# Kernel optimization log

Hardware: AMD Instinct MI355X
Metric: run time of the kernel (lower is better)

The kernel has to match this reference:

```python
import jax, jax.numpy as jnp
import numpy as np

D_MODEL = 1024
N_HEADS = 16
HEAD_DIM = D_MODEL // N_HEADS  # 64
N_T = max(1, int(N_HEADS * 0.25))  # 4 time heads
N_S = N_HEADS - N_T               # 12 space heads
T_DIM = N_T * HEAD_DIM
S_DIM = N_S * HEAD_DIM
B, L = 2, 2048


def setup_inputs() -> dict:
    key = jax.random.key(0)
    ks = jax.random.split(key, 8)
    std = 0.02
    return {
        "x": jax.random.normal(ks[0], (B, L, D_MODEL), dtype=jnp.float32),
        "attention_mask": jnp.zeros((B, 1, 1, L), dtype=jnp.float32),
        # torch nn.Linear weights have shape (out_features, in_features)
        "w_qt": jax.random.normal(ks[1], (T_DIM, D_MODEL), dtype=jnp.float32) * std,
        "w_kt": jax.random.normal(ks[2], (T_DIM, D_MODEL), dtype=jnp.float32) * std,
        "w_qs": jax.random.normal(ks[3], (S_DIM, D_MODEL), dtype=jnp.float32) * std,
        "w_ks": jax.random.normal(ks[4], (S_DIM, D_MODEL), dtype=jnp.float32) * std,
        "w_sigma": jnp.zeros((1,), dtype=jnp.float32),
        "w_v": jax.random.normal(ks[5], (D_MODEL, D_MODEL), dtype=jnp.float32) * std,
        "w_o": jax.random.normal(ks[6], (D_MODEL, D_MODEL), dtype=jnp.float32) * std,
    }


def _heads(x, w, n_h):
    # x:(B,L,D) @ w.T:(D,out) -> (B,L,n_h,d_h) -> (B,n_h,L,d_h)
    b, l, _ = x.shape
    y = jnp.einsum('bld,td->blt', x, w)
    return y.reshape(b, l, n_h, HEAD_DIM).transpose(0, 2, 1, 3)


def reference(x, attention_mask, w_qt, w_kt, w_qs, w_ks, w_sigma, w_v, w_o):
    b, l, _ = x.shape
    scale = np.sqrt(HEAD_DIM).astype(np.float32)
    # F3: time heads (sign-flipped, scaled by learnable sigma) + space heads
    Qt = _heads(x, w_qt, N_T)
    Kt = _heads(x, w_kt, N_T)
    Qs = _heads(x, w_qs, N_S)
    Ks = _heads(x, w_ks, N_S)
    st = jnp.einsum('bhqd,bhkd->bhqk', Qt, Kt)  # (B,N_T,L,L)
    ss = jnp.einsum('bhqd,bhkd->bhqk', Qs, Ks)  # (B,N_S,L,L)
    sigma = jax.nn.sigmoid(w_sigma[0])
    score = jnp.concatenate([-sigma * st, ss], axis=1) / scale  # (B,H,L,L)
    score = score + attention_mask.astype(score.dtype)
    attn_probs = jax.nn.softmax(score, axis=-1).astype(x.dtype)
    # dropout p=0.0 -> identity
    V = _heads(x, w_v, N_HEADS)  # (B,H,L,d_h)
    out = jnp.einsum('bhqk,bhkd->bhqd', attn_probs, V)
    out = out.transpose(0, 2, 1, 3).reshape(b, l, D_MODEL)
    out = jnp.einsum('bld,od->blo', out, w_o)
    return out, attn_probs
```

## Files before the change

### kernel.cpp

```cpp
#include <hip/hip_runtime.h>

typedef __bf16 bf16x8 __attribute__((ext_vector_type(8)));
typedef float f32x4 __attribute__((ext_vector_type(4)));
typedef float f32x16 __attribute__((ext_vector_type(16)));
typedef short short4v __attribute__((ext_vector_type(4)));
typedef unsigned short ushort8 __attribute__((ext_vector_type(8)));
typedef unsigned int uint4v __attribute__((ext_vector_type(4)));

#define AS1 __attribute__((address_space(1)))
#define AS3 __attribute__((address_space(3)))
#define GLL16(g, l) __builtin_amdgcn_global_load_lds((const AS1 void*)(g), (AS3 void*)(l), 16, 0, 0)
#define MFMA16(a, b, c) __builtin_amdgcn_mfma_f32_16x16x32_bf16((a), (b), (c), 0, 0, 0)
#define MFMA32(a, b, c) __builtin_amdgcn_mfma_f32_32x32x16_bf16((a), (b), (c), 0, 0, 0)
#define L2E 1.44269504f

__device__ __forceinline__ unsigned short f2bf(float f) {
  unsigned int u = __builtin_bit_cast(unsigned int, f);
  u = (u + 0x7fffu + ((u >> 16) & 1u)) >> 16;
  return (unsigned short)u;
}

__device__ __forceinline__ unsigned int cvtpk_bf16(float lo, float hi) {
  unsigned int r;
  asm("v_cvt_pk_bf16_f32 %0, %1, %2" : "=v"(r) : "v"(lo), "v"(hi));
  return r;
}

__global__ void convert_kernel(const float* __restrict__ x,
                               const float* __restrict__ w_qt, const float* __restrict__ w_kt,
                               const float* __restrict__ w_qs, const float* __restrict__ w_ks,
                               const float* __restrict__ w_v, const float* __restrict__ w_o,
                               unsigned short* __restrict__ xb, unsigned short* __restrict__ wcat,
                               unsigned short* __restrict__ wob) {
  const int NX = 4096 * 1024, NW = 3072 * 1024, NO = 1024 * 1024;
  int stride = gridDim.x * blockDim.x;
  for (int i = blockIdx.x * blockDim.x + threadIdx.x; i < NX + NW + NO; i += stride) {
    if (i < NX) {
      xb[i] = f2bf(x[i]);
    } else if (i < NX + NW) {
      int j = i - NX;
      int n = j >> 10, k = j & 1023;
      const float* src;
      if (n < 256)        src = w_qt + n * 1024;
      else if (n < 1024)  src = w_qs + (n - 256) * 1024;
      else if (n < 1280)  src = w_kt + (n - 1024) * 1024;
      else if (n < 2048)  src = w_ks + (n - 1280) * 1024;
      else                src = w_v + (n - 2048) * 1024;
      wcat[j] = f2bf(src[k]);
    } else {
      int j = i - NX - NW;
      wob[j] = f2bf(w_o[j]);
    }
  }
}

__global__ __launch_bounds__(256) void gemm_qkv(const unsigned short* __restrict__ A,
                                                const unsigned short* __restrict__ Bw,
                                                const float* __restrict__ amask,
                                                unsigned short* __restrict__ qb,
                                                unsigned short* __restrict__ kfrag,
                                                unsigned short* __restrict__ vfrag) {
  __shared__ unsigned short As[128 * 32];
  __shared__ unsigned short Bs[128 * 32];
  const int t = threadIdx.x;
  const int lane = t & 63, wid = t >> 6;
  const int wm = wid >> 1, wn = wid & 1;
  const int lr = lane & 15, lg = lane >> 4;
  const int m0 = blockIdx.x * 128, n0 = blockIdx.y * 128;
  const int K = 1024;
  f32x4 acc[4][4] = {};
  const unsigned short* gA0 = A + (m0 + (t >> 2)) * K + (t & 3) * 8;
  const unsigned short* gB0 = Bw + (n0 + (t >> 2)) * K + (t & 3) * 8;
  char* lA = (char*)As + wid * 1024;
  char* lB = (char*)Bs + wid * 1024;
  for (int k0 = 0; k0 < K; k0 += 32) {
    __syncthreads();
    GLL16(gA0 + k0, lA);
    GLL16(gA0 + 64 * K + k0, lA + 4096);
    GLL16(gB0 + k0, lB);
    GLL16(gB0 + 64 * K + k0, lB + 4096);
    __syncthreads();
    bf16x8 af[4], bfr[4];
#pragma unroll
    for (int i = 0; i < 4; ++i) {
      af[i] = *(const bf16x8*)&As[(wm * 64 + i * 16 + lr) * 32 + lg * 8];
      bfr[i] = *(const bf16x8*)&Bs[(wn * 64 + i * 16 + lr) * 32 + lg * 8];
    }
#pragma unroll
    for (int i = 0; i < 4; ++i)
#pragma unroll
      for (int j = 0; j < 4; ++j)
        acc[i][j] = MFMA16(af[i], bfr[j], acc[i][j]);
  }
#pragma unroll
  for (int i = 0; i < 4; ++i) {
#pragma unroll
    for (int j = 0; j < 4; ++j) {
      int n = n0 + wn * 64 + j * 16 + lr;
      int mb = m0 + wm * 64 + i * 16 + lg * 4;
      int b = mb >> 11, l = mb & 2047;
      f32x4 v = acc[i][j];
      if (n < 1024) {
        int h = n >> 6, d = n & 63;
#pragma unroll
        for (int r = 0; r < 4; ++r)
          qb[((b * 16 + h) * 2048 + l + r) * 64 + d] = f2bf(v[r]);
      } else if (n < 2048) {
        int nn = n - 1024;
        int h = nn >> 6, d = nn & 63;
        int mfr = d >> 4, hi2 = (d >> 3) & 1, e = d & 7;
#pragma unroll
        for (int r = 0; r < 4; ++r) {
          int lr2 = l + r;
          int cgr = lr2 >> 5, ck = lr2 & 31;
          size_t idx = ((size_t)((b * 16 + h) * 64 + cgr) * 4 + mfr) * 512 + (hi2 * 32 + ck) * 8 + e;
          kfrag[idx] = f2bf(v[r]);
        }
      } else {
        int nn = n - 2048;
        int h = nn >> 6, d = nn & 63;
        int dh = d >> 5, dcol = d & 31;
        int kk = l & 31;
        int kh = kk >> 4, hi2 = (kk >> 3) & 1, i0 = kk & 7;
        const float* mrow = amask + b * 2048 + l;
        size_t idx = ((size_t)((b * 16 + h) * 64 + (l >> 5)) * 4 + (kh * 2 + dh)) * 512
                     + (hi2 * 32 + dcol) * 8 + i0;
        short4v pk;
#pragma unroll
        for (int r = 0; r < 4; ++r)
          pk[r] = (short)f2bf(v[r] * __expf(mrow[r]));
        *(short4v*)&vfrag[idx] = pk;
      }
    }
  }
}

__global__ __launch_bounds__(256, 3) void attn_kernel(const unsigned short* __restrict__ qb,
                                                      const unsigned short* __restrict__ kfrag,
                                                      const unsigned short* __restrict__ vfrag,
                                                      const float* __restrict__ mask,
                                                      const float* __restrict__ w_sigma,
                                                      float* __restrict__ probs,
                                                      unsigned short* __restrict__ ao) {
  __shared__ __align__(16) float pvacc[2048];
  __shared__ float psum[4][32];
  __shared__ float rsum[32];
  const int t = threadIdx.x;
  const int lane = t & 63, w = t >> 6;
  const int col = lane & 31, hi = lane >> 5;
  const int s = blockIdx.x;
  const int bh = (s & 7) * 4 + ((s >> 3) >> 6);
  const int q0 = ((s >> 3) & 63) * 32;
  const int b = bh >> 4, h = bh & 15;
  const float sigma = 1.0f / (1.0f + __expf(-w_sigma[0]));
  const float fac2 = ((h < 4) ? (-sigma * 0.125f) : 0.125f) * L2E;
  const float* maskb = mask + b * 2048;
  const int cg0 = w * 16;

  const unsigned short* kfb = kfrag + (size_t)bh * 131072;
  const unsigned short* vfb = vfrag + (size_t)bh * 131072;

  for (int i = t; i < 2048; i += 256) pvacc[i] = 0.0f;

  bf16x8 qf[4];
  {
    const unsigned short* qp = qb + (size_t)(bh * 2048 + q0 + col) * 64 + hi * 8;
#pragma unroll
    for (int m = 0; m < 4; ++m) qf[m] = *(const bf16x8*)(qp + m * 16);
  }

  float rs[16];
#pragma unroll
  for (int r = 0; r < 16; ++r) rs[r] = 0.f;
  for (int c = 0; c < 16; ++c) {
    int cg = cg0 + c;
    const unsigned short* kp = kfb + (size_t)cg * 2048 + lane * 8;
    bf16x8 kf0 = *(const bf16x8*)(kp);
    bf16x8 kf1 = *(const bf16x8*)(kp + 512);
    bf16x8 kf2 = *(const bf16x8*)(kp + 1024);
    bf16x8 kf3 = *(const bf16x8*)(kp + 1536);
    float mv2 = maskb[cg * 32 + col] * L2E;
    f32x16 sacc = {};
    sacc = MFMA32(qf[0], kf0, sacc);
    sacc = MFMA32(qf[1], kf1, sacc);
    sacc = MFMA32(qf[2], kf2, sacc);
    sacc = MFMA32(qf[3], kf3, sacc);
#pragma unroll
    for (int r = 0; r < 16; ++r) rs[r] += exp2f(sacc[r] * fac2 + mv2);
  }
#pragma unroll
  for (int o = 1; o < 32; o <<= 1)
#pragma unroll
    for (int r = 0; r < 16; ++r) rs[r] += __shfl_xor(rs[r], o);
  if (col == 0) {
#pragma unroll
    for (int r = 0; r < 16; ++r) psum[w][(r & 3) + 8 * (r >> 2) + 4 * hi] = rs[r];
  }
  __syncthreads();
  if (t < 32) rsum[t] = -log2f(psum[0][t] + psum[1][t] + psum[2][t] + psum[3][t]);
  __syncthreads();

  float rws_l[16];
#pragma unroll
  for (int r = 0; r < 16; ++r) rws_l[r] = rsum[(r & 3) + 8 * (r >> 2) + 4 * hi];
  const float rws_t = rsum[col];

  f32x16 oacc0 = {}, oacc1 = {};
  float* pp = probs + (size_t)(bh * 2048 + q0) * 2048;
  for (int c = 0; c < 16; ++c) {
    int cg = cg0 + c;
    const unsigned short* kp = kfb + (size_t)cg * 2048 + lane * 8;
    const unsigned short* vp = vfb + (size_t)cg * 2048 + lane * 8;
    bf16x8 kf0 = *(const bf16x8*)(kp);
    bf16x8 kf1 = *(const bf16x8*)(kp + 512);
    bf16x8 kf2 = *(const bf16x8*)(kp + 1024);
    bf16x8 kf3 = *(const bf16x8*)(kp + 1536);
    bf16x8 vf0 = *(const bf16x8*)(vp);
    bf16x8 vf1 = *(const bf16x8*)(vp + 512);
    bf16x8 vf2 = *(const bf16x8*)(vp + 1024);
    bf16x8 vf3 = *(const bf16x8*)(vp + 1536);
    float mv2 = maskb[cg * 32 + col] * L2E;
    f32x16 sn = {}, st_ = {};
    sn = MFMA32(qf[0], kf0, sn);  st_ = MFMA32(kf0, qf[0], st_);
    sn = MFMA32(qf[1], kf1, sn);  st_ = MFMA32(kf1, qf[1], st_);
    sn = MFMA32(qf[2], kf2, sn);  st_ = MFMA32(kf2, qf[2], st_);
    sn = MFMA32(qf[3], kf3, sn);  st_ = MFMA32(kf3, qf[3], st_);
    float pn[16];
#pragma unroll
    for (int r = 0; r < 16; ++r) pn[r] = exp2f(sn[r] * fac2 + (rws_l[r] + mv2));
    float pt[16];
#pragma unroll
    for (int r = 0; r < 16; ++r) pt[r] = exp2f(fminf(st_[r] * fac2 + rws_t, 60.0f));
    unsigned int A0 = cvtpk_bf16(pt[0], pt[1]),   B0 = cvtpk_bf16(pt[4], pt[5]);
    unsigned int C0 = cvtpk_bf16(pt[2], pt[3]),   D0 = cvtpk_bf16(pt[6], pt[7]);
    unsigned int E0 = cvtpk_bf16(pt[8], pt[9]),   F0 = cvtpk_bf16(pt[12], pt[13]);
    unsigned int G0 = cvtpk_bf16(pt[10], pt[11]), H0 = cvtpk_bf16(pt[14], pt[15]);
    asm("v_permlane32_swap_b32 %0, %1" : "+v"(A0), "+v"(B0));
    asm("v_permlane32_swap_b32 %0, %1" : "+v"(C0), "+v"(D0));
    asm("v_permlane32_swap_b32 %0, %1" : "+v"(E0), "+v"(F0));
    asm("v_permlane32_swap_b32 %0, %1" : "+v"(G0), "+v"(H0));
    uint4v u1; u1[0] = A0; u1[1] = C0; u1[2] = B0; u1[3] = D0;
    uint4v u2; u2[0] = E0; u2[1] = G0; u2[2] = F0; u2[3] = H0;
    bf16x8 frag1 = __builtin_bit_cast(bf16x8, u1);
    bf16x8 frag2 = __builtin_bit_cast(bf16x8, u2);
    oacc0 = MFMA32(frag1, vf0, oacc0);
    oacc1 = MFMA32(frag1, vf1, oacc1);
    oacc0 = MFMA32(frag2, vf2, oacc0);
    oacc1 = MFMA32(frag2, vf3, oacc1);
    float* pr = pp + cg * 32 + col;
#pragma unroll
    for (int r = 0; r < 16; ++r) {
      int row = (r & 3) + 8 * (r >> 2) + 4 * hi;
      __builtin_nontemporal_store(pn[r], pr + (size_t)row * 2048);
    }
  }

  __syncthreads();
#pragma unroll
  for (int r = 0; r < 16; ++r) {
    int row = (r & 3) + 8 * (r >> 2) + 4 * hi;
    atomicAdd(&pvacc[row * 64 + col], oacc0[r]);
    atomicAdd(&pvacc[row * 64 + 32 + col], oacc1[r]);
  }
  __syncthreads();
  {
    int row = t >> 3, c8 = (t & 7) * 8;
    f32x4 v0 = *(const f32x4*)&pvacc[row * 64 + c8];
    f32x4 v1 = *(const f32x4*)&pvacc[row * 64 + c8 + 4];
    ushort8 o;
#pragma unroll
    for (int i = 0; i < 4; ++i) {
      o[i] = f2bf(v0[i]);
      o[i + 4] = f2bf(v1[i]);
    }
    *(ushort8*)&ao[((b * 2048) + q0 + row) * 1024 + h * 64 + c8] = o;
  }
}

__global__ __launch_bounds__(256) void gemm_oproj(const unsigned short* __restrict__ A,
                                                  const unsigned short* __restrict__ Bw,
                                                  float* __restrict__ out) {
  __shared__ unsigned short As[128 * 32];
  __shared__ unsigned short Bs[128 * 32];
  const int t = threadIdx.x;
  const int lane = t & 63, wid = t >> 6;
  const int wm = wid >> 1, wn = wid & 1;
  const int lr = lane & 15, lg = lane >> 4;
  const int m0 = blockIdx.x * 128, n0 = blockIdx.y * 128;
  const int K = 1024;
  f32x4 acc[4][4] = {};
  const unsigned short* gA0 = A + (m0 + (t >> 2)) * K + (t & 3) * 8;
  const unsigned short* gB0 = Bw + (n0 + (t >> 2)) * K + (t & 3) * 8;
  char* lA = (char*)As + wid * 1024;
  char* lB = (char*)Bs + wid * 1024;
  for (int k0 = 0; k0 < K; k0 += 32) {
    __syncthreads();
    GLL16(gA0 + k0, lA);
    GLL16(gA0 + 64 * K + k0, lA + 4096);
    GLL16(gB0 + k0, lB);
    GLL16(gB0 + 64 * K + k0, lB + 4096);
    __syncthreads();
    bf16x8 af[4], bfr[4];
#pragma unroll
    for (int i = 0; i < 4; ++i) {
      af[i] = *(const bf16x8*)&As[(wm * 64 + i * 16 + lr) * 32 + lg * 8];
      bfr[i] = *(const bf16x8*)&Bs[(wn * 64 + i * 16 + lr) * 32 + lg * 8];
    }
#pragma unroll
    for (int i = 0; i < 4; ++i)
#pragma unroll
      for (int j = 0; j < 4; ++j)
        acc[i][j] = MFMA16(af[i], bfr[j], acc[i][j]);
  }
#pragma unroll
  for (int i = 0; i < 4; ++i) {
#pragma unroll
    for (int j = 0; j < 4; ++j) {
      int n = n0 + wn * 64 + j * 16 + lr;
      int mb = m0 + wm * 64 + i * 16 + lg * 4;
#pragma unroll
      for (int r = 0; r < 4; ++r)
        out[(mb + r) * 1024 + n] = acc[i][j][r];
    }
  }
}

extern "C" void kernel_launch(void* const* d_in, const int* in_sizes, int n_in,
                              void* d_out, int out_size, void* d_ws, size_t ws_size,
                              hipStream_t stream) {
  const float* x       = (const float*)d_in[0];
  const float* amask   = (const float*)d_in[1];
  const float* w_qt    = (const float*)d_in[2];
  const float* w_kt    = (const float*)d_in[3];
  const float* w_qs    = (const float*)d_in[4];
  const float* w_ks    = (const float*)d_in[5];
  const float* w_sigma = (const float*)d_in[6];
  const float* w_v     = (const float*)d_in[7];
  const float* w_o     = (const float*)d_in[8];

  char* ws = (char*)d_ws;
  unsigned short* xb    = (unsigned short*)ws;
  unsigned short* wcat  = (unsigned short*)(ws + 8388608);
  unsigned short* wob   = (unsigned short*)(ws + 14680064);
  unsigned short* qb    = (unsigned short*)(ws + 16777216);
  unsigned short* kfrag = (unsigned short*)(ws + 25165824);
  unsigned short* vfrag = (unsigned short*)(ws + 33554432);
  unsigned short* ao    = (unsigned short*)(ws + 41943040);

  float* outp = (float*)d_out;
  float* probs = outp + 4194304;

  convert_kernel<<<2048, 256, 0, stream>>>(x, w_qt, w_kt, w_qs, w_ks, w_v, w_o, xb, wcat, wob);
  gemm_qkv<<<dim3(32, 24), 256, 0, stream>>>(xb, wcat, amask, qb, kfrag, vfrag);
  attn_kernel<<<2048, 256, 0, stream>>>(qb, kfrag, vfrag, amask, w_sigma, probs, ao);
  gemm_oproj<<<dim3(32, 8), 256, 0, stream>>>(ao, wob, outp);
}
```

Measured before the change: 273.0 us.

## Drop duplicate score MFMA, stage probs through LDS for vectorized coalesced stores

```diff
diff --git a/kernel.cpp b/kernel.cpp
--- a/kernel.cpp
+++ b/kernel.cpp
@@ -56,7 +56,6 @@
 
 __global__ __launch_bounds__(256) void gemm_qkv(const unsigned short* __restrict__ A,
                                                 const unsigned short* __restrict__ Bw,
-                                                const float* __restrict__ amask,
                                                 unsigned short* __restrict__ qb,
                                                 unsigned short* __restrict__ kfrag,
                                                 unsigned short* __restrict__ vfrag) {
@@ -122,13 +121,12 @@
         int dh = d >> 5, dcol = d & 31;
         int kk = l & 31;
         int kh = kk >> 4, hi2 = (kk >> 3) & 1, i0 = kk & 7;
-        const float* mrow = amask + b * 2048 + l;
         size_t idx = ((size_t)((b * 16 + h) * 64 + (l >> 5)) * 4 + (kh * 2 + dh)) * 512
                      + (hi2 * 32 + dcol) * 8 + i0;
         short4v pk;
 #pragma unroll
         for (int r = 0; r < 4; ++r)
-          pk[r] = (short)f2bf(v[r] * __expf(mrow[r]));
+          pk[r] = (short)f2bf(v[r]);
         *(short4v*)&vfrag[idx] = pk;
       }
     }
@@ -142,6 +140,7 @@
                                                       const float* __restrict__ w_sigma,
                                                       float* __restrict__ probs,
                                                       unsigned short* __restrict__ ao) {
+  __shared__ __align__(16) char pls[4][4096];
   __shared__ __align__(16) float pvacc[2048];
   __shared__ float psum[4][32];
   __shared__ float rsum[32];
@@ -199,14 +198,13 @@
   __syncthreads();
   if (t < 32) rsum[t] = -log2f(psum[0][t] + psum[1][t] + psum[2][t] + psum[3][t]);
   __syncthreads();
-
-  float rws_l[16];
-#pragma unroll
-  for (int r = 0; r < 16; ++r) rws_l[r] = rsum[(r & 3) + 8 * (r >> 2) + 4 * hi];
   const float rws_t = rsum[col];
 
   f32x16 oacc0 = {}, oacc1 = {};
   float* pp = probs + (size_t)(bh * 2048 + q0) * 2048;
+  char* pl = pls[w];
+  const int rrow = lane >> 3;
+  const int rq = lane & 7;
   for (int c = 0; c < 16; ++c) {
     int cg = cg0 + c;
     const unsigned short* kp = kfb + (size_t)cg * 2048 + lane * 8;
@@ -219,18 +217,26 @@
     bf16x8 vf1 = *(const bf16x8*)(vp + 512);
     bf16x8 vf2 = *(const bf16x8*)(vp + 1024);
     bf16x8 vf3 = *(const bf16x8*)(vp + 1536);
-    float mv2 = maskb[cg * 32 + col] * L2E;
-    f32x16 sn = {}, st_ = {};
-    sn = MFMA32(qf[0], kf0, sn);  st_ = MFMA32(kf0, qf[0], st_);
-    sn = MFMA32(qf[1], kf1, sn);  st_ = MFMA32(kf1, qf[1], st_);
-    sn = MFMA32(qf[2], kf2, sn);  st_ = MFMA32(kf2, qf[2], st_);
-    sn = MFMA32(qf[3], kf3, sn);  st_ = MFMA32(kf3, qf[3], st_);
-    float pn[16];
-#pragma unroll
-    for (int r = 0; r < 16; ++r) pn[r] = exp2f(sn[r] * fac2 + (rws_l[r] + mv2));
+    f32x16 st_ = {};
+    st_ = MFMA32(kf0, qf[0], st_);
+    st_ = MFMA32(kf1, qf[1], st_);
+    st_ = MFMA32(kf2, qf[2], st_);
+    st_ = MFMA32(kf3, qf[3], st_);
+    f32x4 lv[4];
+#pragma unroll
+    for (int g = 0; g < 4; ++g)
+      lv[g] = *(const f32x4*)&maskb[cg * 32 + g * 8 + hi * 4];
     float pt[16];
 #pragma unroll
-    for (int r = 0; r < 16; ++r) pt[r] = exp2f(fminf(st_[r] * fac2 + rws_t, 60.0f));
+    for (int r = 0; r < 16; ++r)
+      pt[r] = exp2f(st_[r] * fac2 + (lv[r >> 2][r & 3] * L2E + rws_t));
+#pragma unroll
+    for (int g = 0; g < 4; ++g) {
+      f32x4 v4;
+      v4[0] = pt[4 * g]; v4[1] = pt[4 * g + 1]; v4[2] = pt[4 * g + 2]; v4[3] = pt[4 * g + 3];
+      int qd = 2 * g + hi;
+      *(f32x4*)(pl + col * 128 + ((qd ^ (col & 7)) << 4)) = v4;
+    }
     unsigned int A0 = cvtpk_bf16(pt[0], pt[1]),   B0 = cvtpk_bf16(pt[4], pt[5]);
     unsigned int C0 = cvtpk_bf16(pt[2], pt[3]),   D0 = cvtpk_bf16(pt[6], pt[7]);
     unsigned int E0 = cvtpk_bf16(pt[8], pt[9]),   F0 = cvtpk_bf16(pt[12], pt[13]);
@@ -247,11 +253,13 @@
     oacc1 = MFMA32(frag1, vf1, oacc1);
     oacc0 = MFMA32(frag2, vf2, oacc0);
     oacc1 = MFMA32(frag2, vf3, oacc1);
-    float* pr = pp + cg * 32 + col;
-#pragma unroll
-    for (int r = 0; r < 16; ++r) {
-      int row = (r & 3) + 8 * (r >> 2) + 4 * hi;
-      __builtin_nontemporal_store(pn[r], pr + (size_t)row * 2048);
+    asm volatile("s_waitcnt lgkmcnt(0)" ::: "memory");
+    float* prow = pp + cg * 32;
+#pragma unroll
+    for (int j = 0; j < 4; ++j) {
+      int q2 = 8 * j + rrow;
+      f32x4 v4 = *(const f32x4*)(pl + q2 * 128 + ((rq ^ (q2 & 7)) << 4));
+      __builtin_nontemporal_store(v4, (f32x4*)(prow + (size_t)q2 * 2048 + rq * 4));
     }
   }
 
@@ -351,7 +359,7 @@
   float* probs = outp + 4194304;
 
   convert_kernel<<<2048, 256, 0, stream>>>(x, w_qt, w_kt, w_qs, w_ks, w_v, w_o, xb, wcat, wob);
-  gemm_qkv<<<dim3(32, 24), 256, 0, stream>>>(xb, wcat, amask, qb, kfrag, vfrag);
+  gemm_qkv<<<dim3(32, 24), 256, 0, stream>>>(xb, wcat, qb, kfrag, vfrag);
   attn_kernel<<<2048, 256, 0, stream>>>(qb, kfrag, vfrag, amask, w_sigma, probs, ao);
   gemm_oproj<<<dim3(32, 8), 256, 0, stream>>>(ao, wob, outp);
 }
```

New measurement: 284.4 us. 1.04x slower.
